# Performance work log

Hardware: AMD Instinct MI355X
Metric: run time of the kernel (lower is better)

Reference implementation:

```python
import jax, jax.numpy as jnp
import numpy as np

B, S, IN, H, OUT = 64, 2048, 256, 128, 3


def setup_inputs() -> dict:
    key = jax.random.key(0)
    ks = jax.random.split(key, 7)
    s_in = 1.0 / np.sqrt(IN)
    s_h = 1.0 / np.sqrt(H)
    return {
        "x": jax.random.normal(ks[0], (B, S, IN), dtype=jnp.float32),
        "W_xh": jax.random.uniform(ks[1], (H, IN), jnp.float32, -s_in, s_in),
        "b_xh": jax.random.uniform(ks[2], (H,), jnp.float32, -s_in, s_in),
        "W_hh": jax.random.uniform(ks[3], (H, H), jnp.float32, -s_h, s_h),
        "b_hh": jax.random.uniform(ks[4], (H,), jnp.float32, -s_h, s_h),
        "b_h": jnp.zeros((H,), dtype=jnp.float32),
        "W_fc": jax.random.uniform(ks[5], (OUT, H), jnp.float32, -s_h, s_h),
        "b_fc": jax.random.uniform(ks[6], (OUT,), jnp.float32, -s_h, s_h),
    }


def reference(x, W_xh, b_xh, W_hh, b_hh, b_h, W_fc, b_fc):
    batch = x.shape[0]
    hidden = W_hh.shape[0]
    # Precompute input projection for all timesteps in one batched matmul: [B,S,H]
    xproj = jnp.einsum("bsi,hi->bsh", x, W_xh) + b_xh
    bias = b_hh + b_h  # fused constant bias per step

    def step(h, xp_t):
        # h: [B,H], xp_t: [B,H]
        h_new = jnp.tanh(xp_t + h @ W_hh.T + bias)
        return h_new, None

    h0 = jnp.zeros((batch, hidden), dtype=x.dtype)
    h_final, _ = jax.lax.scan(step, h0, jnp.swapaxes(xproj, 0, 1))  # scan over S
    return h_final @ W_fc.T + b_fc
```

## Files before the change

kernel.cpp:

```cpp
#include <hip/hip_runtime.h>
#include <hip/hip_bf16.h>
#include <hip/hip_fp16.h>


#define RNN_B   64
#define RNN_S   2048
#define RNN_IN  256
#define RNN_H   128
#define RNN_OUT 3

typedef _Float16 half2v __attribute__((ext_vector_type(2)));
typedef _Float16 half4 __attribute__((ext_vector_type(4)));
typedef _Float16 half8 __attribute__((ext_vector_type(8)));
typedef float f32x4 __attribute__((ext_vector_type(4)));

#if __has_builtin(__builtin_amdgcn_fdot2)
#define FDOT2(a, b, c) __builtin_amdgcn_fdot2((a), (b), (c), false)
#else
#define FDOT2(a, b, c) \
  fmaf((float)(a).x, (float)(b).x, fmaf((float)(a).y, (float)(b).y, (c)))
#endif

__device__ __forceinline__ void block_sync_lds() {
  asm volatile("s_waitcnt lgkmcnt(0)" ::: "memory");
  __builtin_amdgcn_s_barrier();
}

#define XLOADC(SET, KC)                                                       \
  {                                                                           \
    const int _kc = (KC);                                                     \
    _Pragma("unroll")                                                         \
    for (int p = 0; p < 4; ++p) {                                             \
      const int row = lr + 32 * p;                                            \
      SET##a[p] = *(const float4*)&x[(size_t)(m0 + row) * RNN_IN + _kc + lc]; \
      SET##b[p] = *(const float4*)&Wxh[(size_t)row * RNN_IN + _kc + lc];      \
    }                                                                         \
  }

#define XSTORE(SET)                                                 \
  {                                                                 \
    _Pragma("unroll")                                               \
    for (int p = 0; p < 4; ++p) {                                   \
      const int row = lr + 32 * p;                                  \
      half4 ha, hb;                                                 \
      ha.x = (_Float16)SET##a[p].x; ha.y = (_Float16)SET##a[p].y;   \
      ha.z = (_Float16)SET##a[p].z; ha.w = (_Float16)SET##a[p].w;   \
      hb.x = (_Float16)SET##b[p].x; hb.y = (_Float16)SET##b[p].y;   \
      hb.z = (_Float16)SET##b[p].z; hb.w = (_Float16)SET##b[p].w;   \
      *(half4*)&Ash[row][lc] = ha;                                  \
      *(half4*)&Bsh[row][lc] = hb;                                  \
    }                                                               \
  }

#define XCOMPUTE()                                                  \
  {                                                                 \
    half8 af[4], bf[4];                                             \
    _Pragma("unroll")                                               \
    for (int m = 0; m < 4; ++m)                                     \
      af[m] = *(const half8*)&Ash[wr * 64 + m * 16 + fr][fk * 8];   \
    _Pragma("unroll")                                               \
    for (int n = 0; n < 4; ++n)                                     \
      bf[n] = *(const half8*)&Bsh[wc * 64 + n * 16 + fr][fk * 8];   \
    _Pragma("unroll")                                               \
    for (int m = 0; m < 4; ++m)                                     \
      _Pragma("unroll")                                             \
      for (int n = 0; n < 4; ++n)                                   \
        acc[m][n] = __builtin_amdgcn_mfma_f32_16x16x32_f16(         \
            af[m], bf[n], acc[m][n], 0, 0, 0);                      \
  }

__global__ __launch_bounds__(256, 2) void xproj_mfma(
    const float* __restrict__ x, const float* __restrict__ Wxh,
    const float* __restrict__ bxh, float* __restrict__ xp) {
  __shared__ __align__(16) _Float16 Ash[128][40];
  __shared__ __align__(16) _Float16 Bsh[128][40];

  const int tid = threadIdx.x;
  const int m0 = blockIdx.x * 128;
  const int wv = tid >> 6;
  const int lane = tid & 63;
  const int wr = wv >> 1;
  const int wc = wv & 1;
  const int fr = lane & 15;
  const int fk = lane >> 4;

  const int lr = tid >> 3;
  const int lc = (tid & 7) * 4;

  f32x4 acc[4][4];
#pragma unroll
  for (int m = 0; m < 4; ++m)
#pragma unroll
    for (int n = 0; n < 4; ++n) {
      acc[m][n][0] = 0.f; acc[m][n][1] = 0.f;
      acc[m][n][2] = 0.f; acc[m][n][3] = 0.f;
    }

  float4 Aa[4], Ab[4], Ba[4], Bb[4];
  XLOADC(A, 0)

#pragma unroll 1
  for (int kc = 0; kc < RNN_IN; kc += 64) {
    XSTORE(A)
    { const int nk = kc + 32; XLOADC(B, nk < RNN_IN ? nk : RNN_IN - 32) }
    block_sync_lds();
    XCOMPUTE()
    block_sync_lds();
    XSTORE(B)
    { const int nk = kc + 64; XLOADC(A, nk < RNN_IN ? nk : RNN_IN - 32) }
    block_sync_lds();
    XCOMPUTE()
    block_sync_lds();
  }

  float bb[4];
#pragma unroll
  for (int n = 0; n < 4; ++n) bb[n] = bxh[wc * 64 + n * 16 + fr];
#pragma unroll
  for (int m = 0; m < 4; ++m) {
    const size_t rbase = (size_t)(m0 + wr * 64 + m * 16 + 4 * fk);
#pragma unroll
    for (int reg = 0; reg < 4; ++reg) {
      const size_t grow = rbase + reg;
      const size_t bidx = grow >> 11;
      const size_t tidx = grow & 2047;
      float* rowp = &xp[(tidx * RNN_B + bidx) * RNN_H];
#pragma unroll
      for (int n = 0; n < 4; ++n)
        rowp[wc * 64 + n * 16 + fr] = acc[m][n][reg] + bb[n];
    }
  }
}

__device__ __forceinline__ float fast_tanh(float a) {
  const float e = __expf(2.f * a);
  return fmaf(-2.f, __builtin_amdgcn_rcpf(e + 1.f), 1.f);
}

union U8 { half8 v; float f[4]; };

#define WDECL(i) half2v w##i;
#define W_ALL(M) \
  M(0)  M(1)  M(2)  M(3)  M(4)  M(5)  M(6)  M(7)  \
  M(8)  M(9)  M(10) M(11) M(12) M(13) M(14) M(15) \
  M(16) M(17) M(18) M(19) M(20) M(21) M(22) M(23) \
  M(24) M(25) M(26) M(27) M(28) M(29) M(30) M(31)

#define WLOAD2(i0, i1, idx)                                   \
  {                                                           \
    const float4 f = wrow4[idx];                              \
    half2v t; t.x = (_Float16)f.x; t.y = (_Float16)f.y;       \
    w##i0 = t;                                                \
    half2v s; s.x = (_Float16)f.z; s.y = (_Float16)f.w;       \
    w##i1 = s;                                                \
  }
#define W_PAIRS(M) \
  M(0,1,0)    M(2,3,1)    M(4,5,2)    M(6,7,3)    \
  M(8,9,4)    M(10,11,5)  M(12,13,6)  M(14,15,7)  \
  M(16,17,8)  M(18,19,9)  M(20,21,10) M(22,23,11) \
  M(24,25,12) M(26,27,13) M(28,29,14) M(30,31,15)

#define D4(U, wa, wb, wc_, wd)                                   \
  a0 = FDOT2(wa,  __builtin_bit_cast(half2v, (U).f[0]), a0);     \
  a1 = FDOT2(wb,  __builtin_bit_cast(half2v, (U).f[1]), a1);     \
  a2 = FDOT2(wc_, __builtin_bit_cast(half2v, (U).f[2]), a2);     \
  a3 = FDOT2(wd,  __builtin_bit_cast(half2v, (U).f[3]), a3);

#define SSTEP(CUR, NXT, PX, TNEXT)                                    \
  {                                                                   \
    const half8* hp = (const half8*)&hs[CUR][64 * hh];                \
    U8 u0, u1, u2, u3, u4, u5, u6, u7;                                \
    u0.v = hp[0]; u1.v = hp[1]; u2.v = hp[2]; u3.v = hp[3];           \
    u4.v = hp[4]; u5.v = hp[5]; u6.v = hp[6]; u7.v = hp[7];           \
    const float xin = PX;                                             \
    PX = xpb[(size_t)(TNEXT) * (RNN_B * RNN_H)];                      \
    float a0 = 0.f, a1 = 0.f, a2 = 0.f, a3 = 0.f;                     \
    D4(u0, w0,  w1,  w2,  w3)                                         \
    D4(u1, w4,  w5,  w6,  w7)                                         \
    D4(u2, w8,  w9,  w10, w11)                                        \
    D4(u3, w12, w13, w14, w15)                                        \
    D4(u4, w16, w17, w18, w19)                                        \
    D4(u5, w20, w21, w22, w23)                                        \
    D4(u6, w24, w25, w26, w27)                                        \
    D4(u7, w28, w29, w30, w31)                                        \
    float s = (a0 + a1) + (a2 + a3);                                  \
    {                                                                 \
      int tdpp = __builtin_amdgcn_mov_dpp(                            \
          __builtin_bit_cast(int, s), 0xB1, 0xF, 0xF, true);          \
      s += __builtin_bit_cast(float, tdpp);                           \
    }                                                                 \
    const float hv = fast_tanh(bias + xin + s);                       \
    hs[NXT][r] = (_Float16)hv;       \
    hvF = hv;                                                         \
    block_sync_lds();                                                 \
  }

__global__ __launch_bounds__(256, 1) void rnn_scan(
    const float* __restrict__ xq, const float* __restrict__ Whh,
    const float* __restrict__ bhh, const float* __restrict__ bh,
    const float* __restrict__ Wfc, const float* __restrict__ bfc,
    float* __restrict__ out) {
  const int b = blockIdx.x;
  const int tid = threadIdx.x;
  const int wv = tid >> 6;
  const int lane = tid & 63;
  const int r = 32 * wv + (lane >> 1);
  const int hh = lane & 1;

  __shared__ __align__(16) _Float16 hs[2][RNN_H];
  __shared__ float hfin[RNN_H];

  const float4* wrow4 = (const float4*)&Whh[(size_t)r * RNN_H + 64 * hh];
  W_ALL(WDECL)
  W_PAIRS(WLOAD2)

  const float bias = bhh[r] + bh[r];

  if (tid < RNN_H) hs[0][tid] = (_Float16)0.f;
  block_sync_lds();

  const float* xpb = xq + (size_t)b * RNN_H + r;

  float p0 = xpb[(size_t)0 * (RNN_B * RNN_H)];
  float p1 = xpb[(size_t)1 * (RNN_B * RNN_H)];
  float p2 = xpb[(size_t)2 * (RNN_B * RNN_H)];
  float p3 = xpb[(size_t)3 * (RNN_B * RNN_H)];

  float hvF = 0.f;

#pragma unroll 1
  for (int t = 0; t < RNN_S; t += 4) {
    const int n0 = (t + 4 < RNN_S) ? t + 4 : RNN_S - 1;
    const int n1 = (t + 5 < RNN_S) ? t + 5 : RNN_S - 1;
    const int n2 = (t + 6 < RNN_S) ? t + 6 : RNN_S - 1;
    const int n3 = (t + 7 < RNN_S) ? t + 7 : RNN_S - 1;
    SSTEP(0, 1, p0, n0)
    SSTEP(1, 0, p1, n1)
    SSTEP(0, 1, p2, n2)
    SSTEP(1, 0, p3, n3)
  }

  hfin[r] = hvF;
  block_sync_lds();

  if (tid < RNN_OUT) {
    float s = bfc[tid];
#pragma unroll 8
    for (int k = 0; k < RNN_H; ++k)
      s = fmaf(Wfc[(size_t)tid * RNN_H + k], hfin[k], s);
    out[b * RNN_OUT + tid] = s;
  }
}

extern "C" void kernel_launch(void* const* d_in, const int* in_sizes, int n_in,
                              void* d_out, int out_size, void* d_ws, size_t ws_size,
                              hipStream_t stream) {
  const float* x   = (const float*)d_in[0];
  const float* Wxh = (const float*)d_in[1];
  const float* bxh = (const float*)d_in[2];
  const float* Whh = (const float*)d_in[3];
  const float* bhh = (const float*)d_in[4];
  const float* bh  = (const float*)d_in[5];
  const float* Wfc = (const float*)d_in[6];
  const float* bfc = (const float*)d_in[7];
  float* out = (float*)d_out;
  float* xp  = (float*)d_ws;

  xproj_mfma<<<dim3((RNN_B * RNN_S) / 128), dim3(256), 0, stream>>>(x, Wxh, bxh, xp);
  rnn_scan<<<dim3(RNN_B), dim3(256), 0, stream>>>(xp, Whh, bhh, bh, Wfc, bfc, out);
}
```

Measured before the change: 707.2 us.

## Remap scan threads so each quad computes two hidden rows

```diff
diff --git a/kernel.cpp b/kernel.cpp
--- a/kernel.cpp
+++ b/kernel.cpp
@@ -137,6 +137,16 @@
   return fmaf(-2.f, __builtin_amdgcn_rcpf(e + 1.f), 1.f);
 }
 
+__device__ __forceinline__ float quad_sum_dpp(float s) {
+  int t = __builtin_amdgcn_mov_dpp(__builtin_bit_cast(int, s),
+                                   0xB1, 0xF, 0xF, true);
+  s += __builtin_bit_cast(float, t);
+  t = __builtin_amdgcn_mov_dpp(__builtin_bit_cast(int, s),
+                               0x4E, 0xF, 0xF, true);
+  s += __builtin_bit_cast(float, t);
+  return s;
+}
+
 union U8 { half8 v; float f[4]; };
 
 #define WDECL(i) half2v w##i;
@@ -146,52 +156,47 @@
   M(16) M(17) M(18) M(19) M(20) M(21) M(22) M(23) \
   M(24) M(25) M(26) M(27) M(28) M(29) M(30) M(31)
 
-#define WLOAD2(i0, i1, idx)                                   \
+#define WLOAD2(BASE, i0, i1, idx)                             \
   {                                                           \
-    const float4 f = wrow4[idx];                              \
+    const float4 f = BASE[idx];                               \
     half2v t; t.x = (_Float16)f.x; t.y = (_Float16)f.y;       \
     w##i0 = t;                                                \
     half2v s; s.x = (_Float16)f.z; s.y = (_Float16)f.w;       \
     w##i1 = s;                                                \
   }
-#define W_PAIRS(M) \
-  M(0,1,0)    M(2,3,1)    M(4,5,2)    M(6,7,3)    \
-  M(8,9,4)    M(10,11,5)  M(12,13,6)  M(14,15,7)  \
-  M(16,17,8)  M(18,19,9)  M(20,21,10) M(22,23,11) \
-  M(24,25,12) M(26,27,13) M(28,29,14) M(30,31,15)
-
-#define D4(U, wa, wb, wc_, wd)                                   \
-  a0 = FDOT2(wa,  __builtin_bit_cast(half2v, (U).f[0]), a0);     \
-  a1 = FDOT2(wb,  __builtin_bit_cast(half2v, (U).f[1]), a1);     \
-  a2 = FDOT2(wc_, __builtin_bit_cast(half2v, (U).f[2]), a2);     \
-  a3 = FDOT2(wd,  __builtin_bit_cast(half2v, (U).f[3]), a3);
+
+#define D4X(U, wa, wb, wc_, wd, x0, x1, x2, x3)                  \
+  x0 = FDOT2(wa,  __builtin_bit_cast(half2v, (U).f[0]), x0);     \
+  x1 = FDOT2(wb,  __builtin_bit_cast(half2v, (U).f[1]), x1);     \
+  x2 = FDOT2(wc_, __builtin_bit_cast(half2v, (U).f[2]), x2);     \
+  x3 = FDOT2(wd,  __builtin_bit_cast(half2v, (U).f[3]), x3);
 
 #define SSTEP(CUR, NXT, PX, TNEXT)                                    \
   {                                                                   \
-    const half8* hp = (const half8*)&hs[CUR][64 * hh];                \
-    U8 u0, u1, u2, u3, u4, u5, u6, u7;                                \
+    const half8* hp = (const half8*)&hs[CUR][32 * q];                 \
+    U8 u0, u1, u2, u3;                                                \
     u0.v = hp[0]; u1.v = hp[1]; u2.v = hp[2]; u3.v = hp[3];           \
-    u4.v = hp[4]; u5.v = hp[5]; u6.v = hp[6]; u7.v = hp[7];           \
-    const float xin = PX;                                             \
-    PX = xpb[(size_t)(TNEXT) * (RNN_B * RNN_H)];                      \
+    const float xinA = PX.x, xinB = PX.y;                             \
+    PX = *(const float2*)(xpb + (size_t)(TNEXT) * (RNN_B * RNN_H));   \
     float a0 = 0.f, a1 = 0.f, a2 = 0.f, a3 = 0.f;                     \
-    D4(u0, w0,  w1,  w2,  w3)                                         \
-    D4(u1, w4,  w5,  w6,  w7)                                         \
-    D4(u2, w8,  w9,  w10, w11)                                        \
-    D4(u3, w12, w13, w14, w15)                                        \
-    D4(u4, w16, w17, w18, w19)                                        \
-    D4(u5, w20, w21, w22, w23)                                        \
-    D4(u6, w24, w25, w26, w27)                                        \
-    D4(u7, w28, w29, w30, w31)                                        \
-    float s = (a0 + a1) + (a2 + a3);                                  \
-    {                                                                 \
-      int tdpp = __builtin_amdgcn_mov_dpp(                            \
-          __builtin_bit_cast(int, s), 0xB1, 0xF, 0xF, true);          \
-      s += __builtin_bit_cast(float, tdpp);                           \
-    }                                                                 \
-    const float hv = fast_tanh(bias + xin + s);                       \
-    hs[NXT][r] = (_Float16)hv;       \
-    hvF = hv;                                                         \
+    float b0 = 0.f, b1 = 0.f, b2 = 0.f, b3 = 0.f;                     \
+    D4X(u0, w0,  w1,  w2,  w3,  a0, a1, a2, a3)                       \
+    D4X(u1, w4,  w5,  w6,  w7,  a0, a1, a2, a3)                       \
+    D4X(u2, w8,  w9,  w10, w11, a0, a1, a2, a3)                       \
+    D4X(u3, w12, w13, w14, w15, a0, a1, a2, a3)                       \
+    D4X(u0, w16, w17, w18, w19, b0, b1, b2, b3)                       \
+    D4X(u1, w20, w21, w22, w23, b0, b1, b2, b3)                       \
+    D4X(u2, w24, w25, w26, w27, b0, b1, b2, b3)                       \
+    D4X(u3, w28, w29, w30, w31, b0, b1, b2, b3)                       \
+    float sA = (a0 + a1) + (a2 + a3);                                 \
+    float sB = (b0 + b1) + (b2 + b3);                                 \
+    sA = quad_sum_dpp(sA);                                            \
+    sB = quad_sum_dpp(sB);                                            \
+    const float hvA = fast_tanh(biasA + xinA + sA);                   \
+    const float hvB = fast_tanh(biasB + xinB + sB);                   \
+    half2v pk; pk.x = (_Float16)hvA; pk.y = (_Float16)hvB;            \
+    *(half2v*)&hs[NXT][2 * P] = pk;      \
+    hvFA = hvA; hvFB = hvB;                                           \
     block_sync_lds();                                                 \
   }
 
@@ -202,31 +207,40 @@
     float* __restrict__ out) {
   const int b = blockIdx.x;
   const int tid = threadIdx.x;
-  const int wv = tid >> 6;
-  const int lane = tid & 63;
-  const int r = 32 * wv + (lane >> 1);
-  const int hh = lane & 1;
+  const int P = tid >> 2;
+  const int q = tid & 3;
 
   __shared__ __align__(16) _Float16 hs[2][RNN_H];
   __shared__ float hfin[RNN_H];
 
-  const float4* wrow4 = (const float4*)&Whh[(size_t)r * RNN_H + 64 * hh];
+  const float4* wrowA4 =
+      (const float4*)&Whh[(size_t)(2 * P) * RNN_H + 32 * q];
+  const float4* wrowB4 =
+      (const float4*)&Whh[(size_t)(2 * P + 1) * RNN_H + 32 * q];
   W_ALL(WDECL)
-  W_PAIRS(WLOAD2)
-
-  const float bias = bhh[r] + bh[r];
-
-  if (tid < RNN_H) hs[0][tid] = (_Float16)0.f;
+  WLOAD2(wrowA4, 0, 1, 0)   WLOAD2(wrowA4, 2, 3, 1)
+  WLOAD2(wrowA4, 4, 5, 2)   WLOAD2(wrowA4, 6, 7, 3)
+  WLOAD2(wrowA4, 8, 9, 4)   WLOAD2(wrowA4, 10, 11, 5)
+  WLOAD2(wrowA4, 12, 13, 6) WLOAD2(wrowA4, 14, 15, 7)
+  WLOAD2(wrowB4, 16, 17, 0) WLOAD2(wrowB4, 18, 19, 1)
+  WLOAD2(wrowB4, 20, 21, 2) WLOAD2(wrowB4, 22, 23, 3)
+  WLOAD2(wrowB4, 24, 25, 4) WLOAD2(wrowB4, 26, 27, 5)
+  WLOAD2(wrowB4, 28, 29, 6) WLOAD2(wrowB4, 30, 31, 7)
+
+  const float biasA = bhh[2 * P] + bh[2 * P];
+  const float biasB = bhh[2 * P + 1] + bh[2 * P + 1];
+
+  if (tid < 64) ((float*)hs[0])[tid] = 0.f;
   block_sync_lds();
 
-  const float* xpb = xq + (size_t)b * RNN_H + r;
-
-  float p0 = xpb[(size_t)0 * (RNN_B * RNN_H)];
-  float p1 = xpb[(size_t)1 * (RNN_B * RNN_H)];
-  float p2 = xpb[(size_t)2 * (RNN_B * RNN_H)];
-  float p3 = xpb[(size_t)3 * (RNN_B * RNN_H)];
-
-  float hvF = 0.f;
+  const float* xpb = xq + (size_t)b * RNN_H + 2 * P;
+
+  float2 p0 = *(const float2*)(xpb + (size_t)0 * (RNN_B * RNN_H));
+  float2 p1 = *(const float2*)(xpb + (size_t)1 * (RNN_B * RNN_H));
+  float2 p2 = *(const float2*)(xpb + (size_t)2 * (RNN_B * RNN_H));
+  float2 p3 = *(const float2*)(xpb + (size_t)3 * (RNN_B * RNN_H));
+
+  float hvFA = 0.f, hvFB = 0.f;
 
 #pragma unroll 1
   for (int t = 0; t < RNN_S; t += 4) {
@@ -240,7 +254,10 @@
     SSTEP(1, 0, p3, n3)
   }
 
-  hfin[r] = hvF;
+  {
+    float2 hf; hf.x = hvFA; hf.y = hvFB;
+    *(float2*)&hfin[2 * P] = hf;
+  }
   block_sync_lds();
 
   if (tid < RNN_OUT) {
```

Result: slower. 740.1 us (+4.7%).
